# Kernel optimization log

Measured on AMD Instinct MI355X. Metric: run time of the kernel, lower is better.

The kernel has to match this reference:

```python
import jax, jax.numpy as jnp
import numpy as np

B, T, DIN, DOUT = 32, 128, 1024, 1024


def _linear_params(key, din, dout):
    # matches torch nn.Linear default init: U(-1/sqrt(din), 1/sqrt(din))
    kw, kb = jax.random.split(key)
    s = 1.0 / np.sqrt(din)
    W = jax.random.uniform(kw, (dout, din), minval=-s, maxval=s, dtype=jnp.float32)
    b = jax.random.uniform(kb, (dout,), minval=-s, maxval=s, dtype=jnp.float32)
    return W, b


def setup_inputs() -> dict:
    key = jax.random.key(0)
    kx, kz1, kz2, kr1, kr2, kh1, kh2 = jax.random.split(key, 7)
    x = jax.random.normal(kx, (B, T, DIN), dtype=jnp.float32)
    Wz, bz = _linear_params(kz1, DIN, DOUT)   # w_z
    Uz, cz = _linear_params(kz2, DOUT, DOUT)  # u_z
    Wr, br = _linear_params(kr1, DIN, DOUT)   # w_r
    Ur, cr = _linear_params(kr2, DOUT, DOUT)  # u_r
    Wh, bh = _linear_params(kh1, DIN, DOUT)   # w_h
    Uh, ch = _linear_params(kh2, DOUT, DOUT)  # u_h
    return {"x": x, "Wz": Wz, "bz": bz, "Uz": Uz, "cz": cz,
            "Wr": Wr, "br": br, "Ur": Ur, "cr": cr,
            "Wh": Wh, "bh": bh, "Uh": Uh, "ch": ch}


def reference(x, Wz, bz, Uz, cz, Wr, br, Ur, cr, Wh, bh, Uh, ch):
    # manyToManyGRU with simultaneous=True, bias=False, both activations sigmoid.
    # b_z/b_r/b_h are zero buffers (bias=False) and thus omitted.
    batch, seq, _ = x.shape
    dout = Wz.shape[0]
    h0 = jnp.zeros((batch, dout), dtype=x.dtype)

    def step(h, xt):
        z = jax.nn.sigmoid(xt @ Wz.T + bz + h @ Uz.T + cz)
        r = jax.nn.sigmoid(xt @ Wr.T + br + h @ Ur.T + cr)
        h_hat = jax.nn.sigmoid(xt @ Wh.T + bh + (r * h) @ Uh.T + ch)
        h_new = (1.0 - z) * h + z * h_hat
        return h_new, h_new

    _, ys = jax.lax.scan(step, h0, jnp.swapaxes(x, 0, 1))  # ys: (T, B, D)
    # Original torch code cats per-step (B,D) outputs on dim 0 -> (T*B, D)
    # then reshapes to (B, T, D); reproduce that exact memory reinterpretation.
    return ys.reshape(batch, seq, dout)
```

## Files before the change

### kernel.cpp

```cpp
#include <hip/hip_runtime.h>
#include <stdint.h>

typedef unsigned short u16;
typedef unsigned long long u64;
typedef __attribute__((ext_vector_type(8))) short short8;
typedef __attribute__((ext_vector_type(4))) float f32x4;

#define CNT_OFF    0
#define FLAGQ_OFF  16384
#define FLG_OFF    32768
#define H64_OFF    36864
#define ZERO_BYTES (H64_OFF + 65536)
#define RH64_OFF   ZERO_BYTES
#define BS_OFF     (RH64_OFF + 65536)
#define XB_OFF     (1<<20)
#define WB_OFF     (9<<20)
#define WS_FULL    (21u<<20)

__device__ __forceinline__ float bf2f(u16 v) {
    unsigned u = ((unsigned)v) << 16;
    return __builtin_bit_cast(float, u);
}
__device__ __forceinline__ u16 f2bf(float f) {
    unsigned u = __builtin_bit_cast(unsigned, f);
    unsigned r = 0x7fffu + ((u >> 16) & 1u);
    return (u16)((u + r) >> 16);
}
__device__ __forceinline__ float sigm(float x) { return 1.0f / (1.0f + __expf(-x)); }

__device__ __forceinline__ short8 cvt8f(const float* f) {
    short8 r;
#pragma unroll
    for (int j = 0; j < 8; j++) r[j] = (short)f2bf(f[j]);
    return r;
}
__device__ __forceinline__ short8 cvt8any(const void* src, long ei, unsigned isbf) {
    if (isbf) return *(const short8*)((const u16*)src + ei);
    return cvt8f((const float*)src + ei);
}

union Q2 { u64 q[2]; short8 s; };
__device__ __forceinline__ short8 ld_coh8(const u64* p) {
    Q2 u;
    u.q[0] = __hip_atomic_load(p,     __ATOMIC_RELAXED, __HIP_MEMORY_SCOPE_AGENT);
    u.q[1] = __hip_atomic_load(p + 1, __ATOMIC_RELAXED, __HIP_MEMORY_SCOPE_AGENT);
    return u.s;
}

__device__ __forceinline__ void gbar(unsigned* flgs, unsigned e, unsigned nb) {
    __syncthreads();
    const unsigned tid = threadIdx.x;
    if (tid == 0)
        __hip_atomic_store(flgs + blockIdx.x * 16, e,
                           __ATOMIC_RELAXED, __HIP_MEMORY_SCOPE_AGENT);
    if (tid < nb) {
        while (__hip_atomic_load(flgs + tid * 16,
                                 __ATOMIC_RELAXED, __HIP_MEMORY_SCOPE_AGENT) < e)
            __builtin_amdgcn_s_sleep(1);
    }
    __syncthreads();
}

struct Ptrs { const void* p[13]; };

__global__ __launch_bounds__(256) void detect_k(Ptrs ps, unsigned* flags) {
    const u16* a = (const u16*)ps.p[blockIdx.x];
    __shared__ int tot;
    if (threadIdx.x == 0) tot = 0;
    __syncthreads();
    int cnt = 0;
    for (int i = threadIdx.x; i < 1024; i += 256) {
        unsigned u = a[i];
        unsigned e = (u >> 7) & 0xFF;
        cnt += (e == 0 || (e >= 100 && e <= 140)) ? 1 : 0;
    }
    atomicAdd(&tot, cnt);
    __syncthreads();
    if (threadIdx.x == 0) flags[blockIdx.x] = (tot >= 920) ? 1u : 0u;
}

struct SPtrs { const void* x; const void* W[6]; const void* b[6]; };

__global__ __launch_bounds__(256) void stage_k(SPtrs ps, const unsigned* __restrict__ flags,
                                               u16* __restrict__ xb, u16* __restrict__ wb,
                                               float* __restrict__ bs, int do_x) {
    int blk = blockIdx.x, tid = threadIdx.x;
    int xblocks = do_x ? 2048 : 0;
    if (blk < xblocks) {
        long ei = ((long)blk * 256 + tid) * 8;
        *(short8*)(xb + ei) = cvt8any(ps.x, ei, flags[0]);
    } else if (blk < xblocks + 6 * 512) {
        int r = (blk - xblocks) >> 9;
        const int fidx[6] = {1, 3, 5, 7, 9, 11};
        long ei = ((long)((blk - xblocks) & 511) * 256 + tid) * 8;
        *(short8*)(wb + (long)r * 1048576 + ei) = cvt8any(ps.W[r], ei, flags[fidx[r]]);
    } else {
        const int fb[3] = {2, 6, 10}, fc[3] = {4, 8, 12};
        for (int g = 0; g < 3; g++)
            for (int i = tid; i < 1024; i += 256) {
                float b = flags[fb[g]] ? bf2f(((const u16*)ps.b[2 * g])[i])
                                       : ((const float*)ps.b[2 * g])[i];
                float c = flags[fc[g]] ? bf2f(((const u16*)ps.b[2 * g + 1])[i])
                                       : ((const float*)ps.b[2 * g + 1])[i];
                bs[g * 1024 + i] = b + c;
            }
    }
}

__global__ __launch_bounds__(1024, 4) void gru_rec(
    const void* __restrict__ xbase, int xmode,
    const u16* __restrict__ wb, const float* __restrict__ bs,
    u64* __restrict__ h64, u64* __restrict__ rh64,
    const unsigned* __restrict__ flags,
    unsigned* __restrict__ flgs,
    void* __restrict__ out)
{
    const int tid  = threadIdx.x;
    const int lane = tid & 63, wave = tid >> 6;
    const int quad = lane >> 4, ln = lane & 15;
    const int blk  = blockIdx.x;
    const unsigned NB = gridDim.x;

    const unsigned xisbf = xmode ? 1u : flags[0];
    const unsigned outbf = flags[0];

    const int ct = blk >> 1, rt = blk & 1;
    const int R = rt * 16, C0 = ct * 16;

    const int gA  = wave >> 2, kqA = wave & 3;
    const int kb0 = kqA * 256;
    const int wmapA[4] = {3, 2, 1, 0};
    const u16* BwA = wb + (long)wmapA[gA] * 1048576 + (C0 + ln) * 1024 + kb0 + quad * 8;
    const bool hA  = (gA == 0) || (gA == 2);
    const u64* hAq = h64 + (R + ln) * 256 + (kb0 >> 2) + quad * 2;
    const long xAo = ((long)(R + ln) * 128) * 1024 + kb0 + quad * 8;

    const int gB  = wave >> 3, keB = wave & 7;
    const int kb1 = keB * 128;
    const u16* BwB = wb + (long)(gB ? 4 : 5) * 1048576 + (C0 + ln) * 1024 + kb1 + quad * 8;
    const u64* rhq = rh64 + (R + ln) * 256 + (kb1 >> 2) + quad * 2;
    const long xBo = ((long)(R + ln) * 128) * 1024 + kb1 + quad * 8;

    const float bias_z = bs[C0 + ln];
    const float bias_r = bs[1024 + C0 + ln];
    const float bias_h = bs[2048 + C0 + ln];

    __shared__ float sA[16][4][64];
    __shared__ float zt[4][64];
    __shared__ float ht[4][64];
    __shared__ u16   tT[16][20];

    if (wave == 0)
#pragma unroll
        for (int r = 0; r < 4; r++) ht[r][lane] = 0.f;
    __syncthreads();

    const int prow = lane >> 2, pseg = lane & 3;

    for (int t = 0; t < 128; t++) {
        {
            f32x4 acc = (f32x4){0.f, 0.f, 0.f, 0.f};
            const long xo = xAo + (long)t * 1024;
#pragma unroll
            for (int i = 0; i < 8; i++) {
                short8 a = hA ? ld_coh8(hAq + i * 8)
                              : cvt8any(xbase, xo + i * 32, xisbf);
                acc = __builtin_amdgcn_mfma_f32_16x16x32_bf16(
                    a, *(const short8*)(BwA + i * 32), acc, 0, 0, 0);
            }
#pragma unroll
            for (int r = 0; r < 4; r++) sA[wave][r][lane] = acc[r];
        }
        __syncthreads();
        if (wave == 0) {
#pragma unroll
            for (int r = 0; r < 4; r++) {
                float s = bias_r;
#pragma unroll
                for (int w = 0; w < 8; w++) s += sA[w][r][lane];
                float rv = sigm(s);
                tT[quad * 4 + r][ln] = f2bf(rv * ht[r][lane]);
            }
            u64 v = (u64)tT[prow][pseg * 4] | ((u64)tT[prow][pseg * 4 + 1] << 16)
                  | ((u64)tT[prow][pseg * 4 + 2] << 32) | ((u64)tT[prow][pseg * 4 + 3] << 48);
            __hip_atomic_store(&rh64[(R + prow) * 256 + ct * 4 + pseg], v,
                               __ATOMIC_RELAXED, __HIP_MEMORY_SCOPE_AGENT);
        } else if (wave == 1) {
#pragma unroll
            for (int r = 0; r < 4; r++) {
                float s = bias_z;
#pragma unroll
                for (int w = 8; w < 16; w++) s += sA[w][r][lane];
                zt[r][lane] = sigm(s);
            }
        }
        gbar(flgs, 2 * t + 1, NB);
        {
            f32x4 acc = (f32x4){0.f, 0.f, 0.f, 0.f};
            const long xo = xBo + (long)t * 1024;
#pragma unroll
            for (int i = 0; i < 4; i++) {
                short8 a = (gB == 0) ? ld_coh8(rhq + i * 8)
                                     : cvt8any(xbase, xo + i * 32, xisbf);
                acc = __builtin_amdgcn_mfma_f32_16x16x32_bf16(
                    a, *(const short8*)(BwB + i * 32), acc, 0, 0, 0);
            }
#pragma unroll
            for (int r = 0; r < 4; r++) sA[wave][r][lane] = acc[r];
        }
        __syncthreads();
        if (wave == 0) {
#pragma unroll
            for (int r = 0; r < 4; r++) {
                float s = bias_h;
#pragma unroll
                for (int w = 0; w < 16; w++) s += sA[w][r][lane];
                float hh = sigm(s);
                float z  = zt[r][lane];
                float hv = ht[r][lane];
                float hn = (1.0f - z) * hv + z * hh;
                ht[r][lane] = hn;
                u16 hb = f2bf(hn);
                int row = quad * 4 + r;
                tT[row][ln] = hb;
                long oi = ((long)(t * 32) + R + row) * 1024 + C0 + ln;
                if (outbf) ((u16*)out)[oi] = hb;
                else       ((float*)out)[oi] = hn;
            }
            u64 v = (u64)tT[prow][pseg * 4] | ((u64)tT[prow][pseg * 4 + 1] << 16)
                  | ((u64)tT[prow][pseg * 4 + 2] << 32) | ((u64)tT[prow][pseg * 4 + 3] << 48);
            __hip_atomic_store(&h64[(R + prow) * 256 + ct * 4 + pseg], v,
                               __ATOMIC_RELAXED, __HIP_MEMORY_SCOPE_AGENT);
        }
        if (t < 127) gbar(flgs, 2 * t + 2, NB);
    }
}

extern "C" void kernel_launch(void* const* d_in, const int* in_sizes, int n_in,
                              void* d_out, int out_size, void* d_ws, size_t ws_size,
                              hipStream_t stream)
{
    char* ws = (char*)d_ws;
    hipMemsetAsync(d_ws, 0, ZERO_BYTES, stream);

    unsigned* flgs  = (unsigned*)(ws + CNT_OFF);
    unsigned* flags = (unsigned*)(ws + FLG_OFF);
    u64*      h64   = (u64*)(ws + H64_OFF);
    u64*      rh64  = (u64*)(ws + RH64_OFF);
    float*    bs    = (float*)(ws + BS_OFF);
    u16*      xb    = (u16*)(ws + XB_OFF);

    Ptrs dp;
    for (int i = 0; i < 13; i++) dp.p[i] = d_in[i];
    detect_k<<<13, 256, 0, stream>>>(dp, flags);

    SPtrs sp;
    sp.x = d_in[0];
    sp.W[0] = d_in[1];  sp.W[1] = d_in[3];
    sp.W[2] = d_in[5];  sp.W[3] = d_in[7];
    sp.W[4] = d_in[9];  sp.W[5] = d_in[11];
    sp.b[0] = d_in[2];  sp.b[1] = d_in[4];
    sp.b[2] = d_in[6];  sp.b[3] = d_in[8];
    sp.b[4] = d_in[10]; sp.b[5] = d_in[12];

    if (ws_size >= WS_FULL) {
        u16* wbuf = (u16*)(ws + WB_OFF);
        stage_k<<<2048 + 6 * 512 + 1, 256, 0, stream>>>(sp, flags, xb, wbuf, bs, 1);
        gru_rec<<<128, 1024, 0, stream>>>(xb, 1, wbuf, bs, h64, rh64, flags, flgs, d_out);
    } else {
        u16* wbuf = (u16*)(ws + XB_OFF);
        stage_k<<<6 * 512 + 1, 256, 0, stream>>>(sp, flags, xb, wbuf, bs, 0);
        gru_rec<<<128, 1024, 0, stream>>>(d_in[0], 0, wbuf, bs, h64, rh64, flags, flgs, d_out);
    }
}
```

Measured before the change: 1.648 ms.

## Replace global barriers with per-producer dependency flags and double-buffered hidden state

Replaces the two all-block grid barriers per timestep with point-to-point flags. Each wave now waits only on the blocks that produced the h or r*h slices it reads. The hidden state is double-buffered by timestep parity and the second-phase partial sums use a separate shared buffer, so blocks can run ahead without write-after-read hazards. This aims to cut barrier latency and let the x-only MFMA waves proceed without waiting. The risk is subtle memory-ordering bugs, since flags are relaxed atomics with an explicit waitcnt.

```diff
diff --git a/kernel.cpp b/kernel.cpp
--- a/kernel.cpp
+++ b/kernel.cpp
@@ -6,11 +6,11 @@
 typedef __attribute__((ext_vector_type(8))) short short8;
 typedef __attribute__((ext_vector_type(4))) float f32x4;
 
-#define CNT_OFF    0
-#define FLAGQ_OFF  16384
+#define BARF_OFF   0
+#define RHF_OFF    8192
 #define FLG_OFF    32768
 #define H64_OFF    36864
-#define ZERO_BYTES (H64_OFF + 65536)
+#define ZERO_BYTES (H64_OFF + 131072)
 #define RH64_OFF   ZERO_BYTES
 #define BS_OFF     (RH64_OFF + 65536)
 #define XB_OFF     (1<<20)
@@ -46,19 +46,11 @@
     u.q[1] = __hip_atomic_load(p + 1, __ATOMIC_RELAXED, __HIP_MEMORY_SCOPE_AGENT);
     return u.s;
 }
-
-__device__ __forceinline__ void gbar(unsigned* flgs, unsigned e, unsigned nb) {
-    __syncthreads();
-    const unsigned tid = threadIdx.x;
-    if (tid == 0)
-        __hip_atomic_store(flgs + blockIdx.x * 16, e,
-                           __ATOMIC_RELAXED, __HIP_MEMORY_SCOPE_AGENT);
-    if (tid < nb) {
-        while (__hip_atomic_load(flgs + tid * 16,
-                                 __ATOMIC_RELAXED, __HIP_MEMORY_SCOPE_AGENT) < e)
-            __builtin_amdgcn_s_sleep(1);
-    }
-    __syncthreads();
+__device__ __forceinline__ unsigned ld_flag(const unsigned* p) {
+    return __hip_atomic_load(p, __ATOMIC_RELAXED, __HIP_MEMORY_SCOPE_AGENT);
+}
+__device__ __forceinline__ void st_flag(unsigned* p, unsigned v) {
+    __hip_atomic_store(p, v, __ATOMIC_RELAXED, __HIP_MEMORY_SCOPE_AGENT);
 }
 
 struct Ptrs { const void* p[13]; };
@@ -112,14 +104,13 @@
     const u16* __restrict__ wb, const float* __restrict__ bs,
     u64* __restrict__ h64, u64* __restrict__ rh64,
     const unsigned* __restrict__ flags,
-    unsigned* __restrict__ flgs,
+    unsigned* __restrict__ barflg, unsigned* __restrict__ rhflg,
     void* __restrict__ out)
 {
     const int tid  = threadIdx.x;
     const int lane = tid & 63, wave = tid >> 6;
     const int quad = lane >> 4, ln = lane & 15;
     const int blk  = blockIdx.x;
-    const unsigned NB = gridDim.x;
 
     const unsigned xisbf = xmode ? 1u : flags[0];
     const unsigned outbf = flags[0];
@@ -132,7 +123,7 @@
     const int wmapA[4] = {3, 2, 1, 0};
     const u16* BwA = wb + (long)wmapA[gA] * 1048576 + (C0 + ln) * 1024 + kb0 + quad * 8;
     const bool hA  = (gA == 0) || (gA == 2);
-    const u64* hAq = h64 + (R + ln) * 256 + (kb0 >> 2) + quad * 2;
+    const int hAoff = (R + ln) * 256 + (kb0 >> 2) + quad * 2;
     const long xAo = ((long)(R + ln) * 128) * 1024 + kb0 + quad * 8;
 
     const int gB  = wave >> 3, keB = wave & 7;
@@ -141,11 +132,17 @@
     const u64* rhq = rh64 + (R + ln) * 256 + (kb1 >> 2) + quad * 2;
     const long xBo = ((long)(R + ln) * 128) * 1024 + kb1 + quad * 8;
 
+    const unsigned* hwait = barflg + ((((kqA << 4) + (lane & 15)) << 1) | rt) * 16;
+    const unsigned* bw0   = barflg + lane * 16;
+    const unsigned* bw1   = barflg + (lane + 64) * 16;
+    const unsigned* rwait = rhflg + ((((keB << 3) + (lane & 7)) << 1) | rt) * 16;
+
     const float bias_z = bs[C0 + ln];
     const float bias_r = bs[1024 + C0 + ln];
     const float bias_h = bs[2048 + C0 + ln];
 
     __shared__ float sA[16][4][64];
+    __shared__ float sB[16][4][64];
     __shared__ float zt[4][64];
     __shared__ float ht[4][64];
     __shared__ u16   tT[16][20];
@@ -158,12 +155,22 @@
     const int prow = lane >> 2, pseg = lane & 3;
 
     for (int t = 0; t < 128; t++) {
+        if (t) {
+            if (hA) {
+                if (lane < 16)
+                    while (ld_flag(hwait) < (unsigned)t) __builtin_amdgcn_s_sleep(1);
+            } else if (wave == 15) {
+                while (ld_flag(bw0) < (unsigned)t || ld_flag(bw1) < (unsigned)t)
+                    __builtin_amdgcn_s_sleep(1);
+            }
+        }
         {
             f32x4 acc = (f32x4){0.f, 0.f, 0.f, 0.f};
+            const u64* hq = h64 + (t & 1) * 8192 + hAoff;
             const long xo = xAo + (long)t * 1024;
 #pragma unroll
             for (int i = 0; i < 8; i++) {
-                short8 a = hA ? ld_coh8(hAq + i * 8)
+                short8 a = hA ? ld_coh8(hq + i * 8)
                               : cvt8any(xbase, xo + i * 32, xisbf);
                 acc = __builtin_amdgcn_mfma_f32_16x16x32_bf16(
                     a, *(const short8*)(BwA + i * 32), acc, 0, 0, 0);
@@ -185,6 +192,8 @@
                   | ((u64)tT[prow][pseg * 4 + 2] << 32) | ((u64)tT[prow][pseg * 4 + 3] << 48);
             __hip_atomic_store(&rh64[(R + prow) * 256 + ct * 4 + pseg], v,
                                __ATOMIC_RELAXED, __HIP_MEMORY_SCOPE_AGENT);
+            asm volatile("s_waitcnt vmcnt(0)" ::: "memory");
+            if (lane == 0) st_flag(rhflg + blk * 16, (unsigned)(t + 1));
         } else if (wave == 1) {
 #pragma unroll
             for (int r = 0; r < 4; r++) {
@@ -194,7 +203,8 @@
                 zt[r][lane] = sigm(s);
             }
         }
-        gbar(flgs, 2 * t + 1, NB);
+        if (gB == 0 && lane < 8)
+            while (ld_flag(rwait) < (unsigned)(t + 1)) __builtin_amdgcn_s_sleep(1);
         {
             f32x4 acc = (f32x4){0.f, 0.f, 0.f, 0.f};
             const long xo = xBo + (long)t * 1024;
@@ -206,7 +216,7 @@
                     a, *(const short8*)(BwB + i * 32), acc, 0, 0, 0);
             }
 #pragma unroll
-            for (int r = 0; r < 4; r++) sA[wave][r][lane] = acc[r];
+            for (int r = 0; r < 4; r++) sB[wave][r][lane] = acc[r];
         }
         __syncthreads();
         if (wave == 0) {
@@ -214,7 +224,7 @@
             for (int r = 0; r < 4; r++) {
                 float s = bias_h;
 #pragma unroll
-                for (int w = 0; w < 16; w++) s += sA[w][r][lane];
+                for (int w = 0; w < 16; w++) s += sB[w][r][lane];
                 float hh = sigm(s);
                 float z  = zt[r][lane];
                 float hv = ht[r][lane];
@@ -229,10 +239,13 @@
             }
             u64 v = (u64)tT[prow][pseg * 4] | ((u64)tT[prow][pseg * 4 + 1] << 16)
                   | ((u64)tT[prow][pseg * 4 + 2] << 32) | ((u64)tT[prow][pseg * 4 + 3] << 48);
-            __hip_atomic_store(&h64[(R + prow) * 256 + ct * 4 + pseg], v,
+            __hip_atomic_store(&h64[((t + 1) & 1) * 8192 + (R + prow) * 256 + ct * 4 + pseg], v,
                                __ATOMIC_RELAXED, __HIP_MEMORY_SCOPE_AGENT);
         }
-        if (t < 127) gbar(flgs, 2 * t + 2, NB);
+        if (t < 127) {
+            __syncthreads();
+            if (tid == 0) st_flag(barflg + blk * 16, (unsigned)(t + 1));
+        }
     }
 }
 
@@ -243,12 +256,13 @@
     char* ws = (char*)d_ws;
     hipMemsetAsync(d_ws, 0, ZERO_BYTES, stream);
 
-    unsigned* flgs  = (unsigned*)(ws + CNT_OFF);
-    unsigned* flags = (unsigned*)(ws + FLG_OFF);
-    u64*      h64   = (u64*)(ws + H64_OFF);
-    u64*      rh64  = (u64*)(ws + RH64_OFF);
-    float*    bs    = (float*)(ws + BS_OFF);
-    u16*      xb    = (u16*)(ws + XB_OFF);
+    unsigned* barflg = (unsigned*)(ws + BARF_OFF);
+    unsigned* rhflg  = (unsigned*)(ws + RHF_OFF);
+    unsigned* flags  = (unsigned*)(ws + FLG_OFF);
+    u64*      h64    = (u64*)(ws + H64_OFF);
+    u64*      rh64   = (u64*)(ws + RH64_OFF);
+    float*    bs     = (float*)(ws + BS_OFF);
+    u16*      xb     = (u16*)(ws + XB_OFF);
 
     Ptrs dp;
     for (int i = 0; i < 13; i++) dp.p[i] = d_in[i];
@@ -266,10 +280,10 @@
     if (ws_size >= WS_FULL) {
         u16* wbuf = (u16*)(ws + WB_OFF);
         stage_k<<<2048 + 6 * 512 + 1, 256, 0, stream>>>(sp, flags, xb, wbuf, bs, 1);
-        gru_rec<<<128, 1024, 0, stream>>>(xb, 1, wbuf, bs, h64, rh64, flags, flgs, d_out);
+        gru_rec<<<128, 1024, 0, stream>>>(xb, 1, wbuf, bs, h64, rh64, flags, barflg, rhflg, d_out);
     } else {
         u16* wbuf = (u16*)(ws + XB_OFF);
         stage_k<<<6 * 512 + 1, 256, 0, stream>>>(sp, flags, xb, wbuf, bs, 0);
-        gru_rec<<<128, 1024, 0, stream>>>(d_in[0], 0, wbuf, bs, h64, rh64, flags, flgs, d_out);
-    }
-}
+        gru_rec<<<128, 1024, 0, stream>>>(d_in[0], 0, wbuf, bs, h64, rh64, flags, barflg, rhflg, d_out);
+    }
+}
```

Result: slower. 1.702 ms (+3.3%).

## Replace grid barriers with tagged per-word dataflow flags and double-buffered state

Applied to the files above, without the earlier changes.

Removes the two grid-wide barriers per timestep in the persistent GRU kernel. Each 64-bit word of the published h and r*h tiles now carries a 16-bit timestep tag, packing three bf16 values per word, and consumers spin on exactly the words they need. h and rh are double-buffered by timestep parity, and the two stages get separate LDS reduction buffers so a block can run ahead without overwriting data still being read. The intent is to replace global all-to-all synchronization with point-to-point dependencies. The cost is more words to load and poll, extra packing work, and correctness depends on the tag scheme and buffer reuse being race-free.

```diff
diff --git a/kernel.cpp b/kernel.cpp
--- a/kernel.cpp
+++ b/kernel.cpp
@@ -6,16 +6,15 @@
 typedef __attribute__((ext_vector_type(8))) short short8;
 typedef __attribute__((ext_vector_type(4))) float f32x4;
 
-#define CNT_OFF    0
-#define FLAGQ_OFF  16384
-#define FLG_OFF    32768
-#define H64_OFF    36864
-#define ZERO_BYTES (H64_OFF + 65536)
-#define RH64_OFF   ZERO_BYTES
-#define BS_OFF     (RH64_OFF + 65536)
+#define FLG_OFF    0
+#define HM_OFF     4096
+#define RHM_OFF    (HM_OFF + 196608)
+#define ZERO_BYTES (RHM_OFF + 196608)
+#define BS_OFF     ZERO_BYTES
 #define XB_OFF     (1<<20)
 #define WB_OFF     (9<<20)
 #define WS_FULL    (21u<<20)
+#define PAR_STRIDE 12288
 
 __device__ __forceinline__ float bf2f(u16 v) {
     unsigned u = ((unsigned)v) << 16;
@@ -39,26 +38,69 @@
     return cvt8f((const float*)src + ei);
 }
 
-union Q2 { u64 q[2]; short8 s; };
-__device__ __forceinline__ short8 ld_coh8(const u64* p) {
-    Q2 u;
-    u.q[0] = __hip_atomic_load(p,     __ATOMIC_RELAXED, __HIP_MEMORY_SCOPE_AGENT);
-    u.q[1] = __hip_atomic_load(p + 1, __ATOMIC_RELAXED, __HIP_MEMORY_SCOPE_AGENT);
-    return u.s;
-}
-
-__device__ __forceinline__ void gbar(unsigned* flgs, unsigned e, unsigned nb) {
-    __syncthreads();
-    const unsigned tid = threadIdx.x;
-    if (tid == 0)
-        __hip_atomic_store(flgs + blockIdx.x * 16, e,
-                           __ATOMIC_RELAXED, __HIP_MEMORY_SCOPE_AGENT);
-    if (tid < nb) {
-        while (__hip_atomic_load(flgs + tid * 16,
-                                 __ATOMIC_RELAXED, __HIP_MEMORY_SCOPE_AGENT) < e)
-            __builtin_amdgcn_s_sleep(1);
-    }
-    __syncthreads();
+__device__ __forceinline__ u64 ld64(const u64* p) {
+    return __hip_atomic_load(p, __ATOMIC_RELAXED, __HIP_MEMORY_SCOPE_AGENT);
+}
+__device__ __forceinline__ void st64(u64* p, u64 v) {
+    __hip_atomic_store(p, v, __ATOMIC_RELAXED, __HIP_MEMORY_SCOPE_AGENT);
+}
+
+template<int NC>
+__device__ __forceinline__ void poll_chunks(u64* m, const u64* base, u64 want) {
+#pragma unroll
+    for (int i = 0; i < NC; i++) {
+#pragma unroll
+        for (int j = 0; j < 3; j++) m[i * 3 + j] = ld64(base + i * 12 + j);
+    }
+    bool ok = true;
+#pragma unroll
+    for (int q = 0; q < NC * 3; q++) ok &= ((m[q] >> 48) == want);
+    while (!ok) {
+        bool c;
+        do {
+            c = true;
+            __builtin_amdgcn_s_sleep(2);
+#pragma unroll
+            for (int i = 0; i < NC; i++) {
+                u64 w = ld64(base + i * 12);
+                c &= ((w >> 48) == want);
+                m[i * 3] = w;
+            }
+        } while (!c);
+#pragma unroll
+        for (int i = 0; i < NC; i++) {
+            m[i * 3 + 1] = ld64(base + i * 12 + 1);
+            m[i * 3 + 2] = ld64(base + i * 12 + 2);
+        }
+        ok = true;
+#pragma unroll
+        for (int q = 0; q < NC * 3; q++) ok &= ((m[q] >> 48) == want);
+    }
+}
+
+__device__ __forceinline__ short8 asm8(const u64* m) {
+    short8 a;
+    a[0] = (short)(u16)m[0]; a[1] = (short)(u16)(m[0] >> 16); a[2] = (short)(u16)(m[0] >> 32);
+    a[3] = (short)(u16)m[1]; a[4] = (short)(u16)(m[1] >> 16); a[5] = (short)(u16)(m[1] >> 32);
+    a[6] = (short)(u16)m[2]; a[7] = (short)(u16)(m[2] >> 16);
+    return a;
+}
+
+__device__ __forceinline__ void publish_tile(u64* dst, int R, int ct, unsigned tag,
+                                             const u16 (*tT)[20], int lane) {
+#pragma unroll
+    for (int pass = 0; pass < 2; pass++) {
+        int g = lane + pass * 64;
+        if (g < 96) {
+            int lr = g / 6, w = g - lr * 6, oc = w / 3, j = w - oc * 3;
+            int cb = oc * 8 + j * 3;
+            u64 v0 = tT[lr][cb];
+            u64 v1 = tT[lr][cb + 1];
+            u64 v2 = (j == 2) ? 0ull : (u64)tT[lr][cb + 2];
+            u64 word = v0 | (v1 << 16) | (v2 << 32) | ((u64)tag << 48);
+            st64(dst + ((long)(R + lr) * 128 + 2 * ct + oc) * 3 + j, word);
+        }
+    }
 }
 
 struct Ptrs { const void* p[13]; };
@@ -110,16 +152,14 @@
 __global__ __launch_bounds__(1024, 4) void gru_rec(
     const void* __restrict__ xbase, int xmode,
     const u16* __restrict__ wb, const float* __restrict__ bs,
-    u64* __restrict__ h64, u64* __restrict__ rh64,
+    u64* __restrict__ hm, u64* __restrict__ rhm,
     const unsigned* __restrict__ flags,
-    unsigned* __restrict__ flgs,
     void* __restrict__ out)
 {
     const int tid  = threadIdx.x;
     const int lane = tid & 63, wave = tid >> 6;
     const int quad = lane >> 4, ln = lane & 15;
     const int blk  = blockIdx.x;
-    const unsigned NB = gridDim.x;
 
     const unsigned xisbf = xmode ? 1u : flags[0];
     const unsigned outbf = flags[0];
@@ -132,13 +172,13 @@
     const int wmapA[4] = {3, 2, 1, 0};
     const u16* BwA = wb + (long)wmapA[gA] * 1048576 + (C0 + ln) * 1024 + kb0 + quad * 8;
     const bool hA  = (gA == 0) || (gA == 2);
-    const u64* hAq = h64 + (R + ln) * 256 + (kb0 >> 2) + quad * 2;
+    const long hAoff = ((long)(R + ln) * 128 + kqA * 32 + quad) * 3;
     const long xAo = ((long)(R + ln) * 128) * 1024 + kb0 + quad * 8;
 
     const int gB  = wave >> 3, keB = wave & 7;
     const int kb1 = keB * 128;
     const u16* BwB = wb + (long)(gB ? 4 : 5) * 1048576 + (C0 + ln) * 1024 + kb1 + quad * 8;
-    const u64* rhq = rh64 + (R + ln) * 256 + (kb1 >> 2) + quad * 2;
+    const long rhoff = ((long)(R + ln) * 128 + keB * 16 + quad) * 3;
     const long xBo = ((long)(R + ln) * 128) * 1024 + kb1 + quad * 8;
 
     const float bias_z = bs[C0 + ln];
@@ -146,6 +186,7 @@
     const float bias_h = bs[2048 + C0 + ln];
 
     __shared__ float sA[16][4][64];
+    __shared__ float sB[16][4][64];
     __shared__ float zt[4][64];
     __shared__ float ht[4][64];
     __shared__ u16   tT[16][20];
@@ -155,18 +196,23 @@
         for (int r = 0; r < 4; r++) ht[r][lane] = 0.f;
     __syncthreads();
 
-    const int prow = lane >> 2, pseg = lane & 3;
-
     for (int t = 0; t < 128; t++) {
         {
             f32x4 acc = (f32x4){0.f, 0.f, 0.f, 0.f};
-            const long xo = xAo + (long)t * 1024;
-#pragma unroll
-            for (int i = 0; i < 8; i++) {
-                short8 a = hA ? ld_coh8(hAq + i * 8)
-                              : cvt8any(xbase, xo + i * 32, xisbf);
-                acc = __builtin_amdgcn_mfma_f32_16x16x32_bf16(
-                    a, *(const short8*)(BwA + i * 32), acc, 0, 0, 0);
+            if (hA) {
+                u64 m[24];
+                poll_chunks<8>(m, hm + (t & 1) * PAR_STRIDE + hAoff, (u64)t);
+#pragma unroll
+                for (int i = 0; i < 8; i++)
+                    acc = __builtin_amdgcn_mfma_f32_16x16x32_bf16(
+                        asm8(m + i * 3), *(const short8*)(BwA + i * 32), acc, 0, 0, 0);
+            } else {
+                const long xo = xAo + (long)t * 1024;
+#pragma unroll
+                for (int i = 0; i < 8; i++)
+                    acc = __builtin_amdgcn_mfma_f32_16x16x32_bf16(
+                        cvt8any(xbase, xo + i * 32, xisbf),
+                        *(const short8*)(BwA + i * 32), acc, 0, 0, 0);
             }
 #pragma unroll
             for (int r = 0; r < 4; r++) sA[wave][r][lane] = acc[r];
@@ -181,10 +227,7 @@
                 float rv = sigm(s);
                 tT[quad * 4 + r][ln] = f2bf(rv * ht[r][lane]);
             }
-            u64 v = (u64)tT[prow][pseg * 4] | ((u64)tT[prow][pseg * 4 + 1] << 16)
-                  | ((u64)tT[prow][pseg * 4 + 2] << 32) | ((u64)tT[prow][pseg * 4 + 3] << 48);
-            __hip_atomic_store(&rh64[(R + prow) * 256 + ct * 4 + pseg], v,
-                               __ATOMIC_RELAXED, __HIP_MEMORY_SCOPE_AGENT);
+            publish_tile(rhm + (t & 1) * PAR_STRIDE, R, ct, (unsigned)(t + 1), tT, lane);
         } else if (wave == 1) {
 #pragma unroll
             for (int r = 0; r < 4; r++) {
@@ -194,19 +237,25 @@
                 zt[r][lane] = sigm(s);
             }
         }
-        gbar(flgs, 2 * t + 1, NB);
         {
             f32x4 acc = (f32x4){0.f, 0.f, 0.f, 0.f};
-            const long xo = xBo + (long)t * 1024;
-#pragma unroll
-            for (int i = 0; i < 4; i++) {
-                short8 a = (gB == 0) ? ld_coh8(rhq + i * 8)
-                                     : cvt8any(xbase, xo + i * 32, xisbf);
-                acc = __builtin_amdgcn_mfma_f32_16x16x32_bf16(
-                    a, *(const short8*)(BwB + i * 32), acc, 0, 0, 0);
-            }
-#pragma unroll
-            for (int r = 0; r < 4; r++) sA[wave][r][lane] = acc[r];
+            if (gB == 0) {
+                u64 m[12];
+                poll_chunks<4>(m, rhm + (t & 1) * PAR_STRIDE + rhoff, (u64)(t + 1));
+#pragma unroll
+                for (int i = 0; i < 4; i++)
+                    acc = __builtin_amdgcn_mfma_f32_16x16x32_bf16(
+                        asm8(m + i * 3), *(const short8*)(BwB + i * 32), acc, 0, 0, 0);
+            } else {
+                const long xo = xBo + (long)t * 1024;
+#pragma unroll
+                for (int i = 0; i < 4; i++)
+                    acc = __builtin_amdgcn_mfma_f32_16x16x32_bf16(
+                        cvt8any(xbase, xo + i * 32, xisbf),
+                        *(const short8*)(BwB + i * 32), acc, 0, 0, 0);
+            }
+#pragma unroll
+            for (int r = 0; r < 4; r++) sB[wave][r][lane] = acc[r];
         }
         __syncthreads();
         if (wave == 0) {
@@ -214,7 +263,7 @@
             for (int r = 0; r < 4; r++) {
                 float s = bias_h;
 #pragma unroll
-                for (int w = 0; w < 16; w++) s += sA[w][r][lane];
+                for (int w = 0; w < 16; w++) s += sB[w][r][lane];
                 float hh = sigm(s);
                 float z  = zt[r][lane];
                 float hv = ht[r][lane];
@@ -227,12 +276,8 @@
                 if (outbf) ((u16*)out)[oi] = hb;
                 else       ((float*)out)[oi] = hn;
             }
-            u64 v = (u64)tT[prow][pseg * 4] | ((u64)tT[prow][pseg * 4 + 1] << 16)
-                  | ((u64)tT[prow][pseg * 4 + 2] << 32) | ((u64)tT[prow][pseg * 4 + 3] << 48);
-            __hip_atomic_store(&h64[(R + prow) * 256 + ct * 4 + pseg], v,
-                               __ATOMIC_RELAXED, __HIP_MEMORY_SCOPE_AGENT);
-        }
-        if (t < 127) gbar(flgs, 2 * t + 2, NB);
+            publish_tile(hm + ((t + 1) & 1) * PAR_STRIDE, R, ct, (unsigned)(t + 1), tT, lane);
+        }
     }
 }
 
@@ -243,10 +288,9 @@
     char* ws = (char*)d_ws;
     hipMemsetAsync(d_ws, 0, ZERO_BYTES, stream);
 
-    unsigned* flgs  = (unsigned*)(ws + CNT_OFF);
     unsigned* flags = (unsigned*)(ws + FLG_OFF);
-    u64*      h64   = (u64*)(ws + H64_OFF);
-    u64*      rh64  = (u64*)(ws + RH64_OFF);
+    u64*      hm    = (u64*)(ws + HM_OFF);
+    u64*      rhm   = (u64*)(ws + RHM_OFF);
     float*    bs    = (float*)(ws + BS_OFF);
     u16*      xb    = (u16*)(ws + XB_OFF);
 
@@ -266,10 +310,10 @@
     if (ws_size >= WS_FULL) {
         u16* wbuf = (u16*)(ws + WB_OFF);
         stage_k<<<2048 + 6 * 512 + 1, 256, 0, stream>>>(sp, flags, xb, wbuf, bs, 1);
-        gru_rec<<<128, 1024, 0, stream>>>(xb, 1, wbuf, bs, h64, rh64, flags, flgs, d_out);
+        gru_rec<<<128, 1024, 0, stream>>>(xb, 1, wbuf, bs, hm, rhm, flags, d_out);
     } else {
         u16* wbuf = (u16*)(ws + XB_OFF);
         stage_k<<<6 * 512 + 1, 256, 0, stream>>>(sp, flags, xb, wbuf, bs, 0);
-        gru_rec<<<128, 1024, 0, stream>>>(d_in[0], 0, wbuf, bs, h64, rh64, flags, flgs, d_out);
-    }
-}
+        gru_rec<<<128, 1024, 0, stream>>>(d_in[0], 0, wbuf, bs, hm, rhm, flags, d_out);
+    }
+}
```

Measured after the change: 3.888 ms. 136% more time.

## Replicate barrier flags and h/rh state buffers four ways to spread polling traffic

Applied to the files above, without the earlier changes.

Each block now writes its barrier flag to four separate slots, and pollers read the replica chosen by their block index mod 4. The hidden-state and r*h exchange buffers are likewise written to four copies, and each block reads the copy matching its replica index. The aim is to spread cross-block polling and coherent loads over more cache lines or channels, so fewer blocks contend on the same addresses. In exchange, each block does four times as many producer stores per step and the workspace that has to be zeroed grows.

```diff
diff --git a/kernel.cpp b/kernel.cpp
--- a/kernel.cpp
+++ b/kernel.cpp
@@ -7,15 +7,15 @@
 typedef __attribute__((ext_vector_type(4))) float f32x4;
 
 #define CNT_OFF    0
-#define FLAGQ_OFF  16384
-#define FLG_OFF    32768
-#define H64_OFF    36864
-#define ZERO_BYTES (H64_OFF + 65536)
+#define FLG_OFF    131072
+#define BS_OFF     135168
+#define H64_OFF    147456
+#define ZERO_BYTES (H64_OFF + 262144)
 #define RH64_OFF   ZERO_BYTES
-#define BS_OFF     (RH64_OFF + 65536)
 #define XB_OFF     (1<<20)
 #define WB_OFF     (9<<20)
 #define WS_FULL    (21u<<20)
+#define REP_STRIDE 8192
 
 __device__ __forceinline__ float bf2f(u16 v) {
     unsigned u = ((unsigned)v) << 16;
@@ -46,16 +46,24 @@
     u.q[1] = __hip_atomic_load(p + 1, __ATOMIC_RELAXED, __HIP_MEMORY_SCOPE_AGENT);
     return u.s;
 }
+__device__ __forceinline__ unsigned ld_flag(const unsigned* p) {
+    return __hip_atomic_load(p, __ATOMIC_RELAXED, __HIP_MEMORY_SCOPE_AGENT);
+}
+__device__ __forceinline__ void st_flag(unsigned* p, unsigned v) {
+    __hip_atomic_store(p, v, __ATOMIC_RELAXED, __HIP_MEMORY_SCOPE_AGENT);
+}
+__device__ __forceinline__ void st64(u64* p, u64 v) {
+    __hip_atomic_store(p, v, __ATOMIC_RELAXED, __HIP_MEMORY_SCOPE_AGENT);
+}
 
 __device__ __forceinline__ void gbar(unsigned* flgs, unsigned e, unsigned nb) {
     __syncthreads();
     const unsigned tid = threadIdx.x;
-    if (tid == 0)
-        __hip_atomic_store(flgs + blockIdx.x * 16, e,
-                           __ATOMIC_RELAXED, __HIP_MEMORY_SCOPE_AGENT);
+    if (tid < 4)
+        st_flag(flgs + blockIdx.x * 256 + tid * 64, e);
     if (tid < nb) {
-        while (__hip_atomic_load(flgs + tid * 16,
-                                 __ATOMIC_RELAXED, __HIP_MEMORY_SCOPE_AGENT) < e)
+        const unsigned* fp = flgs + tid * 256 + (blockIdx.x & 3) * 64;
+        while (ld_flag(fp) < e)
             __builtin_amdgcn_s_sleep(1);
     }
     __syncthreads();
@@ -120,6 +128,7 @@
     const int quad = lane >> 4, ln = lane & 15;
     const int blk  = blockIdx.x;
     const unsigned NB = gridDim.x;
+    const int rep  = blk & 3;
 
     const unsigned xisbf = xmode ? 1u : flags[0];
     const unsigned outbf = flags[0];
@@ -132,13 +141,13 @@
     const int wmapA[4] = {3, 2, 1, 0};
     const u16* BwA = wb + (long)wmapA[gA] * 1048576 + (C0 + ln) * 1024 + kb0 + quad * 8;
     const bool hA  = (gA == 0) || (gA == 2);
-    const u64* hAq = h64 + (R + ln) * 256 + (kb0 >> 2) + quad * 2;
+    const u64* hAq = h64 + rep * REP_STRIDE + (R + ln) * 256 + (kb0 >> 2) + quad * 2;
     const long xAo = ((long)(R + ln) * 128) * 1024 + kb0 + quad * 8;
 
     const int gB  = wave >> 3, keB = wave & 7;
     const int kb1 = keB * 128;
     const u16* BwB = wb + (long)(gB ? 4 : 5) * 1048576 + (C0 + ln) * 1024 + kb1 + quad * 8;
-    const u64* rhq = rh64 + (R + ln) * 256 + (kb1 >> 2) + quad * 2;
+    const u64* rhq = rh64 + rep * REP_STRIDE + (R + ln) * 256 + (kb1 >> 2) + quad * 2;
     const long xBo = ((long)(R + ln) * 128) * 1024 + kb1 + quad * 8;
 
     const float bias_z = bs[C0 + ln];
@@ -183,8 +192,9 @@
             }
             u64 v = (u64)tT[prow][pseg * 4] | ((u64)tT[prow][pseg * 4 + 1] << 16)
                   | ((u64)tT[prow][pseg * 4 + 2] << 32) | ((u64)tT[prow][pseg * 4 + 3] << 48);
-            __hip_atomic_store(&rh64[(R + prow) * 256 + ct * 4 + pseg], v,
-                               __ATOMIC_RELAXED, __HIP_MEMORY_SCOPE_AGENT);
+            u64* dst = &rh64[(R + prow) * 256 + ct * 4 + pseg];
+#pragma unroll
+            for (int rp = 0; rp < 4; rp++) st64(dst + rp * REP_STRIDE, v);
         } else if (wave == 1) {
 #pragma unroll
             for (int r = 0; r < 4; r++) {
@@ -229,8 +239,9 @@
             }
             u64 v = (u64)tT[prow][pseg * 4] | ((u64)tT[prow][pseg * 4 + 1] << 16)
                   | ((u64)tT[prow][pseg * 4 + 2] << 32) | ((u64)tT[prow][pseg * 4 + 3] << 48);
-            __hip_atomic_store(&h64[(R + prow) * 256 + ct * 4 + pseg], v,
-                               __ATOMIC_RELAXED, __HIP_MEMORY_SCOPE_AGENT);
+            u64* dst = &h64[(R + prow) * 256 + ct * 4 + pseg];
+#pragma unroll
+            for (int rp = 0; rp < 4; rp++) st64(dst + rp * REP_STRIDE, v);
         }
         if (t < 127) gbar(flgs, 2 * t + 2, NB);
     }
@@ -245,9 +256,9 @@
 
     unsigned* flgs  = (unsigned*)(ws + CNT_OFF);
     unsigned* flags = (unsigned*)(ws + FLG_OFF);
+    float*    bs    = (float*)(ws + BS_OFF);
     u64*      h64   = (u64*)(ws + H64_OFF);
     u64*      rh64  = (u64*)(ws + RH64_OFF);
-    float*    bs    = (float*)(ws + BS_OFF);
     u16*      xb    = (u16*)(ws + XB_OFF);
 
     Ptrs dp;
```

Result: no change. 1.632 ms (-1.0%).
